# Kernel tuning notes

Measured on AMD Instinct MI355X. Metric: run time of the kernel, lower is better.

Reference implementation:

```python
import jax, jax.numpy as jnp
import numpy as np


def setup_inputs() -> dict:
    key = jax.random.key(0)
    k1, k2 = jax.random.split(key)
    B, N, M, C = 4, 8192, 8192, 3
    ref = jax.random.normal(k1, (B, N, C), dtype=jnp.float32)
    query = jax.random.normal(k2, (B, M, C), dtype=jnp.float32)
    return {"ref": ref, "query": query, "k": 16}


def reference(ref, query, k):
    # ref:   [B, N, C] reference points
    # query: [B, M, C] query points
    # Squared Euclidean distances via ||q||^2 + ||r||^2 - 2 q.r  -> [B, M, N]
    q_sq = jnp.sum(query * query, axis=-1, keepdims=True)          # [B, M, 1]
    r_sq = jnp.sum(ref * ref, axis=-1)[:, None, :]                 # [B, 1, N]
    cross = jnp.einsum("bmc,bnc->bmn", query, ref)                 # [B, M, N]
    d2 = jnp.maximum(q_sq + r_sq - 2.0 * cross, 0.0)
    # k smallest distances, sorted ascending (knn_cuda convention)
    neg_topk, idx = jax.lax.top_k(-d2, k)                          # [B, M, k]
    dist = jnp.sqrt(-neg_topk)
    return dist, idx
```

## Files before the change

kernel.cpp:

```cpp
#include <hip/hip_runtime.h>


#define TPB 256
#define QPB 32
#define SPL 8
#define KK 16
#define TILE_PTS 512
#define CAP 16
#define TRIG 8

__global__ __launch_bounds__(TPB, 4) void knn_topk_kernel(
    const float* __restrict__ ref, const float* __restrict__ query,
    float* __restrict__ dout, float* __restrict__ iout, int N, int M) {
#pragma clang fp contract(off)
  __shared__ float4 tile[TILE_PTS];
  __shared__ unsigned short si[CAP * TPB];
  __shared__ float md[KK * TPB];

  const int tid = threadIdx.x;
  const int h = tid & (SPL - 1);
  const int qid = blockIdx.x * QPB + (tid >> 3);
  const int b = qid / M;

  const float* qp = query + (size_t)qid * 3;
  const float qx = qp[0], qy = qp[1], qz = qp[2];
  float q2 = (qx * qx + qz * qz) + qy * qy;

  float a[KK];
  int ai[KK];
#pragma unroll
  for (int s = 0; s < KK; ++s) { a[s] = 3.0e38f; ai[s] = 0; }
  float T = 3.0e38f;
  int cnt = 0;

  const float* refb = ref + (size_t)b * N * 3;

  auto insert16 = [&](float d, int ix) {
    bool pc = false;
    float pa = 0.f;
    int pi = 0;
#pragma unroll
    for (int s = 0; s < KK; ++s) {
      float oa = a[s];
      int oi = ai[s];
      bool c = d < oa;
      a[s] = c ? (pc ? pa : d) : oa;
      ai[s] = c ? (pc ? pi : ix) : oi;
      pc = c;
      pa = oa;
      pi = oi;
    }
  };

  auto compact = [&](int tbase) {
    int cm = cnt;
    for (int s = 0; s < cm; ++s) {
      int loc = si[s * TPB + tid];
      float4 p = tile[loc];
      float cr = qx * p.x;
      cr = __builtin_fmaf(qy, p.y, cr);
      cr = __builtin_fmaf(qz, p.z, cr);
      float s2 = q2 + p.w;
      float d2 = __builtin_fmaf(-2.0f, cr, s2);
      float d2c = d2 < 0.f ? 0.f : d2;
      if (d2c < a[KK - 1]) insert16(d2c, tbase + loc);
    }
    cnt = 0;
    float a15 = a[KK - 1];
    float m = fminf(a15, __shfl_xor(a15, 1));
    m = fminf(m, __shfl_xor(m, 2));
    T = fminf(m, __shfl_xor(m, 4));
  };

  const int ntiles = N / TILE_PTS;
  for (int t = 0; t < ntiles; ++t) {
    __syncthreads();
    {
      int pl = tid * 2;
      const float* rp = refb + (size_t)(t * TILE_PTS + pl) * 3;
#pragma unroll
      for (int u = 0; u < 2; ++u) {
        float rx = rp[3 * u + 0];
        float ry = rp[3 * u + 1];
        float rz = rp[3 * u + 2];
        float r2 = (rx * rx + rz * rz) + ry * ry;
        tile[pl + u] = make_float4(rx, ry, rz, r2);
      }
    }
    __syncthreads();
    const int tbase = t * TILE_PTS;
    for (int g = 0; g < TILE_PTS / SPL; g += 8) {
#pragma unroll
      for (int u = 0; u < 8; ++u) {
        const int loc = (g + u) * SPL + h;
        float4 p = tile[loc];
        float cr = qx * p.x;
        cr = __builtin_fmaf(qy, p.y, cr);
        cr = __builtin_fmaf(qz, p.z, cr);
        float s2 = q2 + p.w;
        float d2 = __builtin_fmaf(-2.0f, cr, s2);
        if (d2 <= T) {
          si[cnt * TPB + tid] = (unsigned short)loc;
          cnt++;
        }
      }
      if (__any(cnt >= TRIG)) compact(tbase);
    }
    if (__any(cnt > 0)) compact(tbase);
  }

#pragma unroll
  for (int s = 0; s < KK; ++s) {
    md[s * TPB + tid] = a[s];
    si[s * TPB + tid] = (unsigned short)ai[s];
  }
  __syncthreads();
  if (h == 0) {
    int pp[SPL];
    float hd[SPL];
    int hi[SPL];
#pragma unroll
    for (int j = 0; j < SPL; ++j) {
      pp[j] = 0;
      hd[j] = md[tid + j];
      hi[j] = si[tid + j];
    }
    float* dq = dout + (size_t)qid * KK;
    float* iq = iout + (size_t)qid * KK;
    for (int o = 0; o < KK; ++o) {
      int best = 0;
#pragma unroll
      for (int j = 1; j < SPL; ++j) {
        bool bt = (hd[j] < hd[best]) || (hd[j] == hd[best] && hi[j] < hi[best]);
        if (bt) best = j;
      }
      dq[o] = sqrtf(hd[best]);
      iq[o] = (float)hi[best];
      int np = pp[best] + 1;
      pp[best] = np;
      if (np < KK) {
        hd[best] = md[np * TPB + tid + best];
        hi[best] = si[np * TPB + tid + best];
      } else {
        hd[best] = 3.0e38f;
      }
    }
  }
}

extern "C" void kernel_launch(void* const* d_in, const int* in_sizes, int n_in,
                              void* d_out, int out_size, void* d_ws, size_t ws_size,
                              hipStream_t stream) {
  const float* ref = (const float*)d_in[0];
  const float* query = (const float*)d_in[1];
  const int B = 4, C = 3;
  int N = in_sizes[0] / (B * C);
  int M = in_sizes[1] / (B * C);
  float* dout = (float*)d_out;
  float* iout = dout + (size_t)out_size / 2;
  int totalQ = B * M;
  int blocks = totalQ / QPB;
  knn_topk_kernel<<<blocks, TPB, 0, stream>>>(ref, query, dout, iout, N, M);
}
```

Before: 286.3 us.

## Process two queries per thread with packed float2 distance math

Each thread now handles two query points, reusing each shared-memory tile load across both and computing the two distances with packed 2-wide FMA vectors. The goal is to halve LDS traffic per distance and make use of packed FP32 instructions. In exchange, register pressure roughly doubles (two top-16 lists), shared memory grows by a second candidate index buffer, the block count halves, and compaction runs for both queries whenever either triggers.

```diff
diff --git a/kernel.cpp b/kernel.cpp
--- a/kernel.cpp
+++ b/kernel.cpp
@@ -2,40 +2,52 @@
 
 
 #define TPB 256
-#define QPB 32
+#define QPB 64
 #define SPL 8
 #define KK 16
 #define TILE_PTS 512
 #define CAP 16
 #define TRIG 8
 
+typedef float v2f __attribute__((ext_vector_type(2)));
+
 __global__ __launch_bounds__(TPB, 4) void knn_topk_kernel(
     const float* __restrict__ ref, const float* __restrict__ query,
     float* __restrict__ dout, float* __restrict__ iout, int N, int M) {
 #pragma clang fp contract(off)
   __shared__ float4 tile[TILE_PTS];
-  __shared__ unsigned short si[CAP * TPB];
+  __shared__ unsigned short siA[CAP * TPB];
+  __shared__ unsigned short siB[CAP * TPB];
   __shared__ float md[KK * TPB];
 
   const int tid = threadIdx.x;
   const int h = tid & (SPL - 1);
-  const int qid = blockIdx.x * QPB + (tid >> 3);
-  const int b = qid / M;
-
-  const float* qp = query + (size_t)qid * 3;
-  const float qx = qp[0], qy = qp[1], qz = qp[2];
-  float q2 = (qx * qx + qz * qz) + qy * qy;
-
-  float a[KK];
-  int ai[KK];
-#pragma unroll
-  for (int s = 0; s < KK; ++s) { a[s] = 3.0e38f; ai[s] = 0; }
-  float T = 3.0e38f;
-  int cnt = 0;
+  const int qidA = blockIdx.x * QPB + (tid >> 3);
+  const int qidB = qidA + 32;
+  const int b = qidA / M;
+
+  const float* qpA = query + (size_t)qidA * 3;
+  const float* qpB = query + (size_t)qidB * 3;
+  const float qxA = qpA[0], qyA = qpA[1], qzA = qpA[2];
+  const float qxB = qpB[0], qyB = qpB[1], qzB = qpB[2];
+  const float q2A = (qxA * qxA + qzA * qzA) + qyA * qyA;
+  const float q2B = (qxB * qxB + qzB * qzB) + qyB * qyB;
+  const v2f qxv = {qxA, qxB}, qyv = {qyA, qyB}, qzv = {qzA, qzB};
+  const v2f q2v = {q2A, q2B};
+  const v2f m2v = {-2.0f, -2.0f};
+
+  float aA[KK], aB[KK];
+  int aiA[KK], aiB[KK];
+#pragma unroll
+  for (int s = 0; s < KK; ++s) {
+    aA[s] = 3.0e38f; aiA[s] = 0; aB[s] = 3.0e38f; aiB[s] = 0;
+  }
+  float TA = 3.0e38f, TB = 3.0e38f;
+  int cntA = 0, cntB = 0;
 
   const float* refb = ref + (size_t)b * N * 3;
 
-  auto insert16 = [&](float d, int ix) {
+  auto ins = [&](float (&a)[KK], int (&ai)[KK], float d, int ix) {
     bool pc = false;
     float pa = 0.f;
     int pi = 0;
@@ -52,7 +64,9 @@
     }
   };
 
-  auto compact = [&](int tbase) {
+  auto compactQ = [&](unsigned short* si, int& cnt, float (&a)[KK],
+                      int (&ai)[KK], int tbase, float qx, float qy, float qz,
+                      float q2) {
     int cm = cnt;
     for (int s = 0; s < cm; ++s) {
       int loc = si[s * TPB + tid];
@@ -63,13 +77,15 @@
       float s2 = q2 + p.w;
       float d2 = __builtin_fmaf(-2.0f, cr, s2);
       float d2c = d2 < 0.f ? 0.f : d2;
-      if (d2c < a[KK - 1]) insert16(d2c, tbase + loc);
+      if (d2c < a[KK - 1]) ins(a, ai, d2c, tbase + loc);
     }
     cnt = 0;
-    float a15 = a[KK - 1];
-    float m = fminf(a15, __shfl_xor(a15, 1));
+  };
+
+  auto wmin8 = [&](float x) {
+    float m = fminf(x, __shfl_xor(x, 1));
     m = fminf(m, __shfl_xor(m, 2));
-    T = fminf(m, __shfl_xor(m, 4));
+    return fminf(m, __shfl_xor(m, 4));
   };
 
   const int ntiles = N / TILE_PTS;
@@ -94,25 +110,41 @@
       for (int u = 0; u < 8; ++u) {
         const int loc = (g + u) * SPL + h;
         float4 p = tile[loc];
-        float cr = qx * p.x;
-        cr = __builtin_fmaf(qy, p.y, cr);
-        cr = __builtin_fmaf(qz, p.z, cr);
-        float s2 = q2 + p.w;
-        float d2 = __builtin_fmaf(-2.0f, cr, s2);
-        if (d2 <= T) {
-          si[cnt * TPB + tid] = (unsigned short)loc;
-          cnt++;
+        v2f cr = qxv * p.x;
+        cr = __builtin_elementwise_fma(qyv, (v2f){p.y, p.y}, cr);
+        cr = __builtin_elementwise_fma(qzv, (v2f){p.z, p.z}, cr);
+        v2f s2 = q2v + (v2f){p.w, p.w};
+        v2f d2 = __builtin_elementwise_fma(m2v, cr, s2);
+        if (d2.x <= TA) {
+          siA[cntA * TPB + tid] = (unsigned short)loc;
+          cntA++;
         }
-      }
-      if (__any(cnt >= TRIG)) compact(tbase);
-    }
-    if (__any(cnt > 0)) compact(tbase);
-  }
-
+        if (d2.y <= TB) {
+          siB[cntB * TPB + tid] = (unsigned short)loc;
+          cntB++;
+        }
+      }
+      if (__any(cntA >= TRIG) || __any(cntB >= TRIG)) {
+        compactQ(siA, cntA, aA, aiA, tbase, qxA, qyA, qzA, q2A);
+        compactQ(siB, cntB, aB, aiB, tbase, qxB, qyB, qzB, q2B);
+        TA = wmin8(aA[KK - 1]);
+        TB = wmin8(aB[KK - 1]);
+      }
+    }
+    if (__any(cntA > 0) || __any(cntB > 0)) {
+      compactQ(siA, cntA, aA, aiA, tbase, qxA, qyA, qzA, q2A);
+      compactQ(siB, cntB, aB, aiB, tbase, qxB, qyB, qzB, q2B);
+      TA = wmin8(aA[KK - 1]);
+      TB = wmin8(aB[KK - 1]);
+    }
+  }
+
+  float* dq;
+  float* iq;
 #pragma unroll
   for (int s = 0; s < KK; ++s) {
-    md[s * TPB + tid] = a[s];
-    si[s * TPB + tid] = (unsigned short)ai[s];
+    md[s * TPB + tid] = aA[s];
+    siA[s * TPB + tid] = (unsigned short)aiA[s];
   }
   __syncthreads();
   if (h == 0) {
@@ -123,10 +155,10 @@
     for (int j = 0; j < SPL; ++j) {
       pp[j] = 0;
       hd[j] = md[tid + j];
-      hi[j] = si[tid + j];
-    }
-    float* dq = dout + (size_t)qid * KK;
-    float* iq = iout + (size_t)qid * KK;
+      hi[j] = siA[tid + j];
+    }
+    dq = dout + (size_t)qidA * KK;
+    iq = iout + (size_t)qidA * KK;
     for (int o = 0; o < KK; ++o) {
       int best = 0;
 #pragma unroll
@@ -140,7 +172,45 @@
       pp[best] = np;
       if (np < KK) {
         hd[best] = md[np * TPB + tid + best];
-        hi[best] = si[np * TPB + tid + best];
+        hi[best] = siA[np * TPB + tid + best];
+      } else {
+        hd[best] = 3.0e38f;
+      }
+    }
+  }
+  __syncthreads();
+#pragma unroll
+  for (int s = 0; s < KK; ++s) {
+    md[s * TPB + tid] = aB[s];
+    siA[s * TPB + tid] = (unsigned short)aiB[s];
+  }
+  __syncthreads();
+  if (h == 0) {
+    int pp[SPL];
+    float hd[SPL];
+    int hi[SPL];
+#pragma unroll
+    for (int j = 0; j < SPL; ++j) {
+      pp[j] = 0;
+      hd[j] = md[tid + j];
+      hi[j] = siA[tid + j];
+    }
+    dq = dout + (size_t)qidB * KK;
+    iq = iout + (size_t)qidB * KK;
+    for (int o = 0; o < KK; ++o) {
+      int best = 0;
+#pragma unroll
+      for (int j = 1; j < SPL; ++j) {
+        bool bt = (hd[j] < hd[best]) || (hd[j] == hd[best] && hi[j] < hi[best]);
+        if (bt) best = j;
+      }
+      dq[o] = sqrtf(hd[best]);
+      iq[o] = (float)hi[best];
+      int np = pp[best] + 1;
+      pp[best] = np;
+      if (np < KK) {
+        hd[best] = md[np * TPB + tid + best];
+        hi[best] = siA[np * TPB + tid + best];
       } else {
         hd[best] = 3.0e38f;
       }
```

Result: slower. 358.0 us (+25.0%).

## Pack reference points as SoA pairs and compute distances with packed float2 math

Applied to the files above, without the earlier changes.

Reorganizes the shared-memory tile so each pair of reference points is stored as x0,x1,y0,y1,z0,z1,w0,w1. The distance screen then runs on two points at once with 2-wide vector FMAs, which can map to packed FP32 instructions on CDNA. This is meant to cut the number of instructions and LDS loads in the hot screening loop. The candidate buffer capacity grows from 16 to 24 to absorb up to 16 candidates per trigger window, which costs more LDS and may lower occupancy.

```diff
diff --git a/kernel.cpp b/kernel.cpp
--- a/kernel.cpp
+++ b/kernel.cpp
@@ -6,14 +6,17 @@
 #define SPL 8
 #define KK 16
 #define TILE_PTS 512
-#define CAP 16
+#define NPAIR (TILE_PTS / 2)
+#define CAP 24
 #define TRIG 8
+
+typedef float v2f __attribute__((ext_vector_type(2)));
 
 __global__ __launch_bounds__(TPB, 4) void knn_topk_kernel(
     const float* __restrict__ ref, const float* __restrict__ query,
     float* __restrict__ dout, float* __restrict__ iout, int N, int M) {
 #pragma clang fp contract(off)
-  __shared__ float4 tile[TILE_PTS];
+  __shared__ float tp[NPAIR * 8];
   __shared__ unsigned short si[CAP * TPB];
   __shared__ float md[KK * TPB];
 
@@ -24,7 +27,10 @@
 
   const float* qp = query + (size_t)qid * 3;
   const float qx = qp[0], qy = qp[1], qz = qp[2];
-  float q2 = (qx * qx + qz * qz) + qy * qy;
+  const float q2 = (qx * qx + qz * qz) + qy * qy;
+  const v2f qxv = {qx, qx}, qyv = {qy, qy}, qzv = {qz, qz};
+  const v2f q2v = {q2, q2};
+  const v2f m2v = {-2.0f, -2.0f};
 
   float a[KK];
   int ai[KK];
@@ -35,7 +41,7 @@
 
   const float* refb = ref + (size_t)b * N * 3;
 
-  auto insert16 = [&](float d, int ix) {
+  auto ins = [&](float d, int ix) {
     bool pc = false;
     float pa = 0.f;
     int pi = 0;
@@ -56,14 +62,16 @@
     int cm = cnt;
     for (int s = 0; s < cm; ++s) {
       int loc = si[s * TPB + tid];
-      float4 p = tile[loc];
-      float cr = qx * p.x;
-      cr = __builtin_fmaf(qy, p.y, cr);
-      cr = __builtin_fmaf(qz, p.z, cr);
-      float s2 = q2 + p.w;
+      int P = loc >> 1, e = loc & 1;
+      const float* pb = &tp[P * 8];
+      float px = pb[0 + e], py = pb[2 + e], pz = pb[4 + e], pw = pb[6 + e];
+      float cr = qx * px;
+      cr = __builtin_fmaf(qy, py, cr);
+      cr = __builtin_fmaf(qz, pz, cr);
+      float s2 = q2 + pw;
       float d2 = __builtin_fmaf(-2.0f, cr, s2);
       float d2c = d2 < 0.f ? 0.f : d2;
-      if (d2c < a[KK - 1]) insert16(d2c, tbase + loc);
+      if (d2c < a[KK - 1]) ins(d2c, tbase + loc);
     }
     cnt = 0;
     float a15 = a[KK - 1];
@@ -76,32 +84,38 @@
   for (int t = 0; t < ntiles; ++t) {
     __syncthreads();
     {
-      int pl = tid * 2;
-      const float* rp = refb + (size_t)(t * TILE_PTS + pl) * 3;
-#pragma unroll
-      for (int u = 0; u < 2; ++u) {
-        float rx = rp[3 * u + 0];
-        float ry = rp[3 * u + 1];
-        float rz = rp[3 * u + 2];
-        float r2 = (rx * rx + rz * rz) + ry * ry;
-        tile[pl + u] = make_float4(rx, ry, rz, r2);
-      }
+      const float* rp = refb + (size_t)(t * TILE_PTS + 2 * tid) * 3;
+      float x0 = rp[0], y0 = rp[1], z0 = rp[2];
+      float x1 = rp[3], y1 = rp[4], z1 = rp[5];
+      float w0 = (x0 * x0 + z0 * z0) + y0 * y0;
+      float w1 = (x1 * x1 + z1 * z1) + y1 * y1;
+      float4* pb = (float4*)&tp[tid * 8];
+      pb[0] = make_float4(x0, x1, y0, y1);
+      pb[1] = make_float4(z0, z1, w0, w1);
     }
     __syncthreads();
     const int tbase = t * TILE_PTS;
-    for (int g = 0; g < TILE_PTS / SPL; g += 8) {
+    for (int g = 0; g < NPAIR / SPL; g += 8) {
 #pragma unroll
       for (int u = 0; u < 8; ++u) {
-        const int loc = (g + u) * SPL + h;
-        float4 p = tile[loc];
-        float cr = qx * p.x;
-        cr = __builtin_fmaf(qy, p.y, cr);
-        cr = __builtin_fmaf(qz, p.z, cr);
-        float s2 = q2 + p.w;
-        float d2 = __builtin_fmaf(-2.0f, cr, s2);
-        if (d2 <= T) {
-          si[cnt * TPB + tid] = (unsigned short)loc;
-          cnt++;
+        const int P = (g + u) * SPL + h;
+        const v2f* pb = (const v2f*)&tp[P * 8];
+        v2f px = pb[0], py = pb[1], pz = pb[2], pw = pb[3];
+        v2f cr = qxv * px;
+        cr = __builtin_elementwise_fma(qyv, py, cr);
+        cr = __builtin_elementwise_fma(qzv, pz, cr);
+        v2f s2 = q2v + pw;
+        v2f d2 = __builtin_elementwise_fma(m2v, cr, s2);
+        if (fminf(d2.x, d2.y) <= T) {
+          int loc = P * 2;
+          if (d2.x <= T) {
+            si[cnt * TPB + tid] = (unsigned short)loc;
+            cnt++;
+          }
+          if (d2.y <= T) {
+            si[cnt * TPB + tid] = (unsigned short)(loc + 1);
+            cnt++;
+          }
         }
       }
       if (__any(cnt >= TRIG)) compact(tbase);
```

After: 298.9 us. 1.04x slower.
